# Kernel tuning notes

Hardware: AMD Instinct MI355X
Metric: run time of the kernel (lower is better)

The kernel has to match this reference:

```python
import jax, jax.numpy as jnp
import numpy as np

EMBED_DIM = 1024
NUM_HEADS = 16


def setup_inputs() -> dict:
    key = jax.random.key(0)
    kq, kk, kv = jax.random.split(key, 3)
    N, L, S, E = 4, 2048, 2048, EMBED_DIM
    return {
        "query": jax.random.normal(kq, (N, L, E), dtype=jnp.float32),
        "key": jax.random.normal(kk, (N, S, E), dtype=jnp.float32),
        "value": jax.random.normal(kv, (N, S, E), dtype=jnp.float32),
        "is_causal": 1,
    }


def reference(query, key, value, is_causal):
    N, L, E = query.shape
    _, S, E_v = value.shape
    H = NUM_HEADS
    dh = E // H
    dh_v = E_v // H
    # (N, H, L, dh) layout
    q = query.reshape(N, L, H, dh).transpose(0, 2, 1, 3)
    k = key.reshape(N, S, H, dh).transpose(0, 2, 1, 3)
    v = value.reshape(N, S, H, dh_v).transpose(0, 2, 1, 3)

    scale = 1.0 / np.sqrt(dh).astype(np.float32)
    # full LxS score matrix, as in the original (non-flash)
    scores = jnp.einsum('nhld,nhsd->nhls', q, k) * scale
    if is_causal:
        causal = jnp.tril(jnp.ones((L, S), dtype=bool))  # True = allowed
        scores = jnp.where(causal, scores, jnp.float32(-jnp.inf))
    attn_weight = jax.nn.softmax(scores, axis=-1)  # (N,H,L,S)
    y = jnp.einsum('nhls,nhsd->nhld', attn_weight, v)
    y = y.transpose(0, 2, 1, 3).reshape(N, L, E_v)
    return (y, attn_weight)
```

## Files before the change

### kernel.cpp

```cpp
#include <hip/hip_runtime.h>
#include <math.h>
#include <stdint.h>

#define N_B 4
#define N_H 16
#define L_Q 2048
#define L_K 2048
#define E_D 1024
#define DH  64
#define QB  128
#define KB  64
#define NT  512
#define NQT (L_Q / QB)
#define NKT (L_K / KB)
#define LDP  72
#define LDPV 68

typedef _Float16 f16x2 __attribute__((ext_vector_type(2)));
typedef _Float16 f16x4 __attribute__((ext_vector_type(4)));
typedef _Float16 f16x8 __attribute__((ext_vector_type(8)));
typedef float    f32x4 __attribute__((ext_vector_type(4)));

__device__ __forceinline__ f16x4 pk4(float a, float b, float c, float d) {
    f16x2 lo = __builtin_bit_cast(f16x2, __builtin_amdgcn_cvt_pkrtz(a, b));
    f16x2 hi = __builtin_bit_cast(f16x2, __builtin_amdgcn_cvt_pkrtz(c, d));
    f16x4 r; r[0] = lo[0]; r[1] = lo[1]; r[2] = hi[0]; r[3] = hi[1];
    return r;
}

__device__ __forceinline__ void gload16(const _Float16* g, _Float16* l) {
    __builtin_amdgcn_global_load_lds(
        (const __attribute__((address_space(1))) void*)g,
        (__attribute__((address_space(3))) void*)l, 16, 0, 0);
}

__global__ __launch_bounds__(256)
void cvt_qk(const float* __restrict__ Q, const float* __restrict__ K,
            _Float16* __restrict__ Qh, _Float16* __restrict__ Kh)
{
    size_t i = ((size_t)blockIdx.x * 256 + threadIdx.x) * 8;
    float4 a = *(const float4*)(Q + i);
    float4 b = *(const float4*)(Q + i + 4);
    *(f16x4*)(Qh + i)     = pk4(a.x, a.y, a.z, a.w);
    *(f16x4*)(Qh + i + 4) = pk4(b.x, b.y, b.z, b.w);
    float4 c = *(const float4*)(K + i);
    float4 d = *(const float4*)(K + i + 4);
    *(f16x4*)(Kh + i)     = pk4(c.x, c.y, c.z, c.w);
    *(f16x4*)(Kh + i + 4) = pk4(d.x, d.y, d.z, d.w);
}

__global__ __launch_bounds__(256)
void cvt_vt(const float* __restrict__ V, _Float16* __restrict__ Vt)
{
    __shared__ _Float16 T[64][72];
    const int bid = blockIdx.x;
    const int st  = bid & 31;
    const int nh  = bid >> 5;
    const int n   = nh >> 4;
    const int h   = nh & 15;
    const int t   = threadIdx.x;
    const float* Vb = V + ((size_t)(n * L_K + st * 64)) * E_D + h * DH;
    #pragma unroll
    for (int i = 0; i < 4; ++i) {
        int lin = t + i * 256;
        int s = lin >> 4, d = (lin & 15) * 4;
        float4 v = *(const float4*)(Vb + (size_t)s * E_D + d);
        T[d + 0][s] = (_Float16)v.x; T[d + 1][s] = (_Float16)v.y;
        T[d + 2][s] = (_Float16)v.z; T[d + 3][s] = (_Float16)v.w;
    }
    __syncthreads();
    _Float16* Ob = Vt + ((size_t)nh * DH) * L_K + st * 64;
    #pragma unroll
    for (int j = 0; j < 2; ++j) {
        int lin = t + j * 256;
        int d = lin >> 3, sc = (lin & 7) * 8;
        *(f16x8*)(Ob + (size_t)d * L_K + sc) = *(const f16x8*)&T[d][sc];
    }
}

__global__ __launch_bounds__(NT)
void mha_main(const _Float16* __restrict__ Qh, const _Float16* __restrict__ Kh,
              const _Float16* __restrict__ Vth, const int* __restrict__ causp,
              float* __restrict__ Yg, float* __restrict__ Wg)
{
    __shared__ __attribute__((aligned(16))) _Float16 KsL[2][KB * DH];
    __shared__ __attribute__((aligned(16))) _Float16 VsL[2][DH * KB];
    __shared__ __attribute__((aligned(16))) _Float16 Ps[QB][LDP];
    __shared__ float linv[QB];

    const int tid  = threadIdx.x;
    const int lane = tid & 63;
    const int wid  = tid >> 6;
    const int bid0 = blockIdx.x;
    const int bid  = ((bid0 & 7) << 7) + (bid0 >> 3);
    const int qt   = bid & (NQT - 1);
    const int nh   = bid >> 4;
    const int q0   = qt * QB;
    const int n    = nh >> 4;
    const int h    = nh & 15;
    const bool causal = (*causp) != 0;
    const float scale = 0.125f;

    const int lrow = lane & 15;
    const int g    = lane >> 4;
    const int rb   = wid * 16;
    const int rsub = g * 4;
    const int kt_end = causal ? (2 * qt + 2) : NKT;

    float*  Ybase = Yg + ((size_t)(n * L_Q + q0)) * E_D + h * DH;
    float*  Wbase = Wg + ((size_t)nh * L_Q + q0) * L_K;

    const int srow = wid * 8 + (lane >> 3);
    const int scol = (((lane & 7) ^ ((lane >> 3) & 7)) << 3);
    const _Float16* Ksrc0 = Kh  + ((size_t)(n * L_K) + srow) * E_D + h * DH + scol;
    const _Float16* Vsrc0 = Vth + ((size_t)nh * DH + srow) * L_K + scol;

    const int swz = (lrow & 7) << 4;
    const int cb0 = ((g * 16) ^ swz) >> 1;
    const int cb1 = ((64 + g * 16) ^ swz) >> 1;

    const _Float16* Qrow = Qh + ((size_t)(n * L_Q + q0 + rb + lrow)) * E_D + h * DH;
    const f16x8 qf0 = *(const f16x8*)(Qrow + g * 8);
    const f16x8 qf1 = *(const f16x8*)(Qrow + 32 + g * 8);

    #define STAGE_K(b, kt) gload16(Ksrc0 + (size_t)(kt) * KB * E_D, &KsL[b][wid * 512])
    #define STAGE_V(b, kt) gload16(Vsrc0 + (size_t)(kt) * KB,       &VsL[b][wid * 512])
    #define FRAG(buf, tc, half) (*(const f16x8*)&(buf)[(size_t)((tc) * 16 + lrow) * 64 + ((half) ? cb1 : cb0)])

    float l_part = 0.0f;
    STAGE_K(0, 0);
    __syncthreads();
    for (int kt = 0; kt < kt_end; ++kt) {
        const int cur = kt & 1;
        if (kt + 1 < kt_end) STAGE_K(cur ^ 1, kt + 1);

        f32x4 acc[4] = {};
        #pragma unroll
        for (int tc = 0; tc < 4; ++tc) {
            acc[tc] = __builtin_amdgcn_mfma_f32_16x16x32_f16(FRAG(KsL[cur], tc, 0), qf0, acc[tc], 0, 0, 0);
            acc[tc] = __builtin_amdgcn_mfma_f32_16x16x32_f16(FRAG(KsL[cur], tc, 1), qf1, acc[tc], 0, 0, 0);
        }
        const bool dm = causal && (kt >= 2 * qt);
        const int krel = (kt - 2 * qt) * 64;
        #pragma unroll
        for (int tc = 0; tc < 4; ++tc) {
            #pragma unroll
            for (int i = 0; i < 4; ++i) {
                float v = acc[tc][i] * scale;
                bool ok = !dm || (krel + tc * 16 + rsub + i <= rb + lrow);
                l_part += ok ? __expf(v) : 0.0f;
            }
        }
        __syncthreads();
    }
    l_part += __shfl_xor(l_part, 16);
    l_part += __shfl_xor(l_part, 32);
    const float inv_l = 1.0f / l_part;
    linv[rb + lrow] = inv_l;

    f32x4 o[4] = {};
    STAGE_K(0, 0);
    STAGE_V(0, 0);
    __syncthreads();

    float winv[4];
    #pragma unroll
    for (int j = 0; j < 4; ++j) winv[j] = linv[rb + (lane >> 4) + 4 * j];

    for (int kt = 0; kt < kt_end; ++kt) {
        const int cur = kt & 1;
        if (kt + 1 < kt_end) { STAGE_K(cur ^ 1, kt + 1); STAGE_V(cur ^ 1, kt + 1); }

        f32x4 acc[4] = {};
        #pragma unroll
        for (int tc = 0; tc < 4; ++tc) {
            acc[tc] = __builtin_amdgcn_mfma_f32_16x16x32_f16(FRAG(KsL[cur], tc, 0), qf0, acc[tc], 0, 0, 0);
            acc[tc] = __builtin_amdgcn_mfma_f32_16x16x32_f16(FRAG(KsL[cur], tc, 1), qf1, acc[tc], 0, 0, 0);
        }

        const bool dm = causal && (kt >= 2 * qt);
        const int krel = (kt - 2 * qt) * 64;
        #pragma unroll
        for (int tc = 0; tc < 4; ++tc) {
            float v, p0, p1, p2, p3;
            v = acc[tc][0] * scale;
            p0 = (!dm || (krel + tc * 16 + rsub + 0 <= rb + lrow)) ? __expf(v) : 0.0f;
            v = acc[tc][1] * scale;
            p1 = (!dm || (krel + tc * 16 + rsub + 1 <= rb + lrow)) ? __expf(v) : 0.0f;
            v = acc[tc][2] * scale;
            p2 = (!dm || (krel + tc * 16 + rsub + 2 <= rb + lrow)) ? __expf(v) : 0.0f;
            v = acc[tc][3] * scale;
            p3 = (!dm || (krel + tc * 16 + rsub + 3 <= rb + lrow)) ? __expf(v) : 0.0f;
            *(f16x4*)&Ps[rb + lrow][tc * 16 + rsub] = pk4(p0, p1, p2, p3);
        }

        f16x8 pf0 = *(const f16x8*)&Ps[rb + lrow][0 + g * 8];
        f16x8 pf1 = *(const f16x8*)&Ps[rb + lrow][32 + g * 8];
        #pragma unroll
        for (int tc = 0; tc < 4; ++tc) {
            o[tc] = __builtin_amdgcn_mfma_f32_16x16x32_f16(FRAG(VsL[cur], tc, 0), pf0, o[tc], 0, 0, 0);
            o[tc] = __builtin_amdgcn_mfma_f32_16x16x32_f16(FRAG(VsL[cur], tc, 1), pf1, o[tc], 0, 0, 0);
        }

        {
            float* Wt = Wbase + (size_t)kt * KB;
            const int c0 = (lane & 15) * 4;
            #pragma unroll
            for (int j = 0; j < 4; ++j) {
                const int rl = rb + (lane >> 4) + 4 * j;
                f16x4 pv = *(const f16x4*)&Ps[rl][c0];
                const float s = winv[j];
                float4 wv = make_float4((float)pv[0] * s, (float)pv[1] * s,
                                        (float)pv[2] * s, (float)pv[3] * s);
                *(float4*)(Wt + (size_t)rl * L_K + c0) = wv;
            }
        }

        __builtin_amdgcn_sched_barrier(0);
        asm volatile("s_waitcnt vmcnt(4) lgkmcnt(0)" ::: "memory");
        __builtin_amdgcn_s_barrier();
        __builtin_amdgcn_sched_barrier(0);
    }

    #pragma unroll
    for (int tc = 0; tc < 4; ++tc) {
        float4 yv = make_float4(o[tc][0] * inv_l, o[tc][1] * inv_l,
                                o[tc][2] * inv_l, o[tc][3] * inv_l);
        *(float4*)(Ybase + (size_t)(rb + lrow) * E_D + tc * 16 + rsub) = yv;
    }

    if (causal && kt_end < NKT) {
        const int c0 = kt_end * KB;
        const int rem4 = (L_K - c0) >> 2;
        const float4 z = make_float4(0.f, 0.f, 0.f, 0.f);
        for (int r = 0; r < QB; ++r) {
            float* row = Wbase + (size_t)r * L_K + c0;
            for (int c4 = tid; c4 < rem4; c4 += NT) {
                *(float4*)(row + c4 * 4) = z;
            }
        }
    }
    #undef STAGE_K
    #undef STAGE_V
    #undef FRAG
}

__global__ __launch_bounds__(256)
void mha_fwd_fallback(const float* __restrict__ Qg, const float* __restrict__ Kg,
                      const float* __restrict__ Vg, const int* __restrict__ causp,
                      float* __restrict__ Yg, float* __restrict__ Wg)
{
    __shared__ __attribute__((aligned(16))) _Float16 Qs[64][LDP];
    __shared__ __attribute__((aligned(16))) _Float16 Ks[64][LDP];
    __shared__ __attribute__((aligned(16))) _Float16 Psf[64][LDP];
    __shared__ __attribute__((aligned(16))) _Float16 Vt[DH][LDPV];

    const int tid  = threadIdx.x;
    const int lane = tid & 63;
    const int wid  = tid >> 6;
    const int bid  = blockIdx.x;
    const int qt   = bid & 31;
    const int nh   = bid >> 5;
    const int q0   = qt * 64;
    const int n    = nh >> 4;
    const int h    = nh & 15;
    const bool causal = (*causp) != 0;
    const float scale = 0.125f;

    const float* Qbase = Qg + ((size_t)(n * L_Q + q0)) * E_D + h * DH;
    const float* Kbase = Kg + ((size_t)n * L_K) * E_D + h * DH;
    const float* Vbase = Vg + ((size_t)n * L_K) * E_D + h * DH;
    float*       Ybase = Yg + ((size_t)(n * L_Q + q0)) * E_D + h * DH;
    float*       Wbase = Wg + ((size_t)nh * L_Q + q0) * L_K;

    const int lrow = lane & 15;
    const int lk   = (lane >> 4) * 8;
    const int rb   = wid * 16;
    const int rsub = (lane >> 4) * 4;
    const int kt_end = causal ? (qt + 1) : NKT;

    #pragma unroll
    for (int i = 0; i < 4; ++i) {
        int lin = tid + i * 256;
        int r = lin >> 4;
        int c = (lin & 15) * 4;
        float4 qv = *(const float4*)(Qbase + (size_t)r * E_D + c);
        *(f16x4*)&Qs[r][c] = pk4(qv.x, qv.y, qv.z, qv.w);
    }
    __syncthreads();
    const f16x8 qf0 = *(const f16x8*)&Qs[rb + lrow][lk];
    const f16x8 qf1 = *(const f16x8*)&Qs[rb + lrow][32 + lk];

    float l_part = 0.0f;
    for (int kt = 0; kt < kt_end; ++kt) {
        const float* Kt = Kbase + (size_t)kt * KB * E_D;
        __syncthreads();
        #pragma unroll
        for (int i = 0; i < 4; ++i) {
            int lin = tid + i * 256;
            int r = lin >> 4;
            int c = (lin & 15) * 4;
            float4 kv = *(const float4*)(Kt + (size_t)r * E_D + c);
            *(f16x4*)&Ks[r][c] = pk4(kv.x, kv.y, kv.z, kv.w);
        }
        __syncthreads();
        f32x4 acc[4] = {};
        #pragma unroll
        for (int tc = 0; tc < 4; ++tc) {
            f16x8 a0 = *(const f16x8*)&Ks[tc * 16 + lrow][lk];
            f16x8 a1 = *(const f16x8*)&Ks[tc * 16 + lrow][32 + lk];
            acc[tc] = __builtin_amdgcn_mfma_f32_16x16x32_f16(a0, qf0, acc[tc], 0, 0, 0);
            acc[tc] = __builtin_amdgcn_mfma_f32_16x16x32_f16(a1, qf1, acc[tc], 0, 0, 0);
        }
        const bool dm = causal && (kt == qt);
        #pragma unroll
        for (int tc = 0; tc < 4; ++tc) {
            #pragma unroll
            for (int i = 0; i < 4; ++i) {
                float v = acc[tc][i] * scale;
                bool ok = !dm || (tc * 16 + rsub + i <= rb + lrow);
                l_part += ok ? __expf(v) : 0.0f;
            }
        }
    }
    l_part += __shfl_xor(l_part, 16);
    l_part += __shfl_xor(l_part, 32);
    const float inv_l = 1.0f / l_part;

    f32x4 o[4] = {};
    for (int kt = 0; kt < kt_end; ++kt) {
        const float* Kt  = Kbase + (size_t)kt * KB * E_D;
        const float* Vtg = Vbase + (size_t)kt * KB * E_D;
        __syncthreads();
        #pragma unroll
        for (int i = 0; i < 4; ++i) {
            int lin = tid + i * 256;
            int r = lin >> 4;
            int c = (lin & 15) * 4;
            float4 kv = *(const float4*)(Kt + (size_t)r * E_D + c);
            *(f16x4*)&Ks[r][c] = pk4(kv.x, kv.y, kv.z, kv.w);
            int d   = lin & 63;
            int kk0 = (lin >> 6) * 4;
            float v0 = Vtg[(size_t)(kk0 + 0) * E_D + d];
            float v1 = Vtg[(size_t)(kk0 + 1) * E_D + d];
            float v2 = Vtg[(size_t)(kk0 + 2) * E_D + d];
            float v3 = Vtg[(size_t)(kk0 + 3) * E_D + d];
            *(f16x4*)&Vt[d][kk0] = pk4(v0, v1, v2, v3);
        }
        __syncthreads();
        f32x4 acc[4] = {};
        #pragma unroll
        for (int tc = 0; tc < 4; ++tc) {
            f16x8 a0 = *(const f16x8*)&Ks[tc * 16 + lrow][lk];
            f16x8 a1 = *(const f16x8*)&Ks[tc * 16 + lrow][32 + lk];
            acc[tc] = __builtin_amdgcn_mfma_f32_16x16x32_f16(a0, qf0, acc[tc], 0, 0, 0);
            acc[tc] = __builtin_amdgcn_mfma_f32_16x16x32_f16(a1, qf1, acc[tc], 0, 0, 0);
        }
        const bool dm = causal && (kt == qt);
        float* Wrow = Wbase + (size_t)(rb + lrow) * L_K + kt * KB;
        #pragma unroll
        for (int tc = 0; tc < 4; ++tc) {
            float v, p0, p1, p2, p3;
            v = acc[tc][0] * scale;
            p0 = (!dm || (tc * 16 + rsub + 0 <= rb + lrow)) ? __expf(v) : 0.0f;
            v = acc[tc][1] * scale;
            p1 = (!dm || (tc * 16 + rsub + 1 <= rb + lrow)) ? __expf(v) : 0.0f;
            v = acc[tc][2] * scale;
            p2 = (!dm || (tc * 16 + rsub + 2 <= rb + lrow)) ? __expf(v) : 0.0f;
            v = acc[tc][3] * scale;
            p3 = (!dm || (tc * 16 + rsub + 3 <= rb + lrow)) ? __expf(v) : 0.0f;
            float4 wv = make_float4(p0 * inv_l, p1 * inv_l, p2 * inv_l, p3 * inv_l);
            *(float4*)(Wrow + tc * 16 + rsub) = wv;
            *(f16x4*)&Psf[rb + lrow][tc * 16 + rsub] = pk4(p0, p1, p2, p3);
        }
        f16x8 pf0 = *(const f16x8*)&Psf[rb + lrow][lk];
        f16x8 pf1 = *(const f16x8*)&Psf[rb + lrow][32 + lk];
        #pragma unroll
        for (int tc = 0; tc < 4; ++tc) {
            f16x4 t0 = *(const f16x4*)&Vt[tc * 16 + lrow][lk];
            f16x4 t1 = *(const f16x4*)&Vt[tc * 16 + lrow][lk + 4];
            f16x8 a0 = __builtin_shufflevector(t0, t1, 0, 1, 2, 3, 4, 5, 6, 7);
            f16x4 t2 = *(const f16x4*)&Vt[tc * 16 + lrow][32 + lk];
            f16x4 t3 = *(const f16x4*)&Vt[tc * 16 + lrow][32 + lk + 4];
            f16x8 a1 = __builtin_shufflevector(t2, t3, 0, 1, 2, 3, 4, 5, 6, 7);
            o[tc] = __builtin_amdgcn_mfma_f32_16x16x32_f16(a0, pf0, o[tc], 0, 0, 0);
            o[tc] = __builtin_amdgcn_mfma_f32_16x16x32_f16(a1, pf1, o[tc], 0, 0, 0);
        }
    }
    #pragma unroll
    for (int tc = 0; tc < 4; ++tc) {
        float4 yv = make_float4(o[tc][0] * inv_l, o[tc][1] * inv_l,
                                o[tc][2] * inv_l, o[tc][3] * inv_l);
        *(float4*)(Ybase + (size_t)(rb + lrow) * E_D + tc * 16 + rsub) = yv;
    }
    if (causal && kt_end < NKT) {
        const int c0 = kt_end * KB;
        const int rem4 = (L_K - c0) >> 2;
        const float4 z = make_float4(0.f, 0.f, 0.f, 0.f);
        for (int r = 0; r < 64; ++r) {
            float* row = Wbase + (size_t)r * L_K + c0;
            for (int c4 = tid; c4 < rem4; c4 += 256) {
                *(float4*)(row + c4 * 4) = z;
            }
        }
    }
}

extern "C" void kernel_launch(void* const* d_in, const int* in_sizes, int n_in,
                              void* d_out, int out_size, void* d_ws, size_t ws_size,
                              hipStream_t stream) {
    const float* Q  = (const float*)d_in[0];
    const float* K  = (const float*)d_in[1];
    const float* V  = (const float*)d_in[2];
    const int* caus = (const int*)d_in[3];
    float* Y = (float*)d_out;
    float* W = (float*)d_out + (size_t)N_B * L_Q * E_D;

    const size_t elems = (size_t)N_B * L_Q * E_D;
    const size_t need  = 3 * elems * sizeof(_Float16);

    if (ws_size >= need) {
        _Float16* Qh = (_Float16*)d_ws;
        _Float16* Kh = Qh + elems;
        _Float16* Vt = Kh + elems;
        hipLaunchKernelGGL(cvt_qk, dim3(elems / (256 * 8)), dim3(256), 0, stream, Q, K, Qh, Kh);
        hipLaunchKernelGGL(cvt_vt, dim3(N_B * N_H * (L_K / 64)), dim3(256), 0, stream, V, Vt);
        hipLaunchKernelGGL(mha_main, dim3(N_B * N_H * NQT), dim3(NT), 0, stream,
                           Qh, Kh, Vt, caus, Y, W);
    } else {
        hipLaunchKernelGGL(mha_fwd_fallback, dim3(N_B * N_H * 32), dim3(256), 0, stream,
                           Q, K, V, caus, Y, W);
    }
}
```

Measured before the change: 328.3 us.

## Reverse q-tile order, pair K tiles in row-sum pass, use nontemporal stores

Three changes. Query tiles are now assigned in reverse, so the causal blocks with the most K tiles get scheduled first, which helps load balance. The first (row-sum) pass stages two K tiles per barrier, borrowing the V buffer as a second slot, which halves the number of barriers. The output and attention-weight stores, including the zero fill, become nontemporal to cut cache pollution on the large write stream. The pairing assumes kt_end is even; under the causal setting it is 2*qt+2, and in the non-causal case it is 32.

```diff
diff --git a/kernel.cpp b/kernel.cpp
--- a/kernel.cpp
+++ b/kernel.cpp
@@ -93,7 +93,7 @@
     const int wid  = tid >> 6;
     const int bid0 = blockIdx.x;
     const int bid  = ((bid0 & 7) << 7) + (bid0 >> 3);
-    const int qt   = bid & (NQT - 1);
+    const int qt   = (NQT - 1) - (bid & (NQT - 1));
     const int nh   = bid >> 4;
     const int q0   = qt * QB;
     const int n    = nh >> 4;
@@ -124,31 +124,45 @@
     const f16x8 qf1 = *(const f16x8*)(Qrow + 32 + g * 8);
 
     #define STAGE_K(b, kt) gload16(Ksrc0 + (size_t)(kt) * KB * E_D, &KsL[b][wid * 512])
+    #define STAGE_KV(b, kt) gload16(Ksrc0 + (size_t)(kt) * KB * E_D, &VsL[b][wid * 512])
     #define STAGE_V(b, kt) gload16(Vsrc0 + (size_t)(kt) * KB,       &VsL[b][wid * 512])
     #define FRAG(buf, tc, half) (*(const f16x8*)&(buf)[(size_t)((tc) * 16 + lrow) * 64 + ((half) ? cb1 : cb0)])
 
     float l_part = 0.0f;
-    STAGE_K(0, 0);
-    __syncthreads();
-    for (int kt = 0; kt < kt_end; ++kt) {
-        const int cur = kt & 1;
-        if (kt + 1 < kt_end) STAGE_K(cur ^ 1, kt + 1);
-
-        f32x4 acc[4] = {};
-        #pragma unroll
-        for (int tc = 0; tc < 4; ++tc) {
-            acc[tc] = __builtin_amdgcn_mfma_f32_16x16x32_f16(FRAG(KsL[cur], tc, 0), qf0, acc[tc], 0, 0, 0);
-            acc[tc] = __builtin_amdgcn_mfma_f32_16x16x32_f16(FRAG(KsL[cur], tc, 1), qf1, acc[tc], 0, 0, 0);
-        }
-        const bool dm = causal && (kt >= 2 * qt);
-        const int krel = (kt - 2 * qt) * 64;
-        #pragma unroll
-        for (int tc = 0; tc < 4; ++tc) {
+    {
+        const int np = kt_end >> 1;
+        STAGE_K(0, 0);
+        STAGE_KV(0, 1);
+        for (int p = 0; p < np; ++p) {
+            __builtin_amdgcn_sched_barrier(0);
+            asm volatile("s_waitcnt vmcnt(0) lgkmcnt(0)" ::: "memory");
+            __builtin_amdgcn_s_barrier();
+            __builtin_amdgcn_sched_barrier(0);
+            if (p + 1 < np) {
+                STAGE_K((p + 1) & 1, 2 * p + 2);
+                STAGE_KV((p + 1) & 1, 2 * p + 3);
+            }
             #pragma unroll
-            for (int i = 0; i < 4; ++i) {
-                float v = acc[tc][i] * scale;
-                bool ok = !dm || (krel + tc * 16 + rsub + i <= rb + lrow);
-                l_part += ok ? __expf(v) : 0.0f;
+            for (int half = 0; half < 2; ++half) {
+                const int kt = 2 * p + half;
+                const _Float16* Kc = half ? &VsL[p & 1][0] : &KsL[p & 1][0];
+                f32x4 acc[4] = {};
+                #pragma unroll
+                for (int tc = 0; tc < 4; ++tc) {
+                    acc[tc] = __builtin_amdgcn_mfma_f32_16x16x32_f16(FRAG(Kc, tc, 0), qf0, acc[tc], 0, 0, 0);
+                    acc[tc] = __builtin_amdgcn_mfma_f32_16x16x32_f16(FRAG(Kc, tc, 1), qf1, acc[tc], 0, 0, 0);
+                }
+                const bool dm = causal && (kt >= 2 * qt);
+                const int krel = (kt - 2 * qt) * 64;
+                #pragma unroll
+                for (int tc = 0; tc < 4; ++tc) {
+                    #pragma unroll
+                    for (int i = 0; i < 4; ++i) {
+                        float v = acc[tc][i] * scale;
+                        bool ok = !dm || (krel + tc * 16 + rsub + i <= rb + lrow);
+                        l_part += ok ? __expf(v) : 0.0f;
+                    }
+                }
             }
         }
         __syncthreads();
@@ -210,9 +224,9 @@
                 const int rl = rb + (lane >> 4) + 4 * j;
                 f16x4 pv = *(const f16x4*)&Ps[rl][c0];
                 const float s = winv[j];
-                float4 wv = make_float4((float)pv[0] * s, (float)pv[1] * s,
-                                        (float)pv[2] * s, (float)pv[3] * s);
-                *(float4*)(Wt + (size_t)rl * L_K + c0) = wv;
+                f32x4 wv = { (float)pv[0] * s, (float)pv[1] * s,
+                             (float)pv[2] * s, (float)pv[3] * s };
+                __builtin_nontemporal_store(wv, (f32x4*)(Wt + (size_t)rl * L_K + c0));
             }
         }
 
@@ -224,23 +238,24 @@
 
     #pragma unroll
     for (int tc = 0; tc < 4; ++tc) {
-        float4 yv = make_float4(o[tc][0] * inv_l, o[tc][1] * inv_l,
-                                o[tc][2] * inv_l, o[tc][3] * inv_l);
-        *(float4*)(Ybase + (size_t)(rb + lrow) * E_D + tc * 16 + rsub) = yv;
+        f32x4 yv = { o[tc][0] * inv_l, o[tc][1] * inv_l,
+                     o[tc][2] * inv_l, o[tc][3] * inv_l };
+        __builtin_nontemporal_store(yv, (f32x4*)(Ybase + (size_t)(rb + lrow) * E_D + tc * 16 + rsub));
     }
 
     if (causal && kt_end < NKT) {
         const int c0 = kt_end * KB;
         const int rem4 = (L_K - c0) >> 2;
-        const float4 z = make_float4(0.f, 0.f, 0.f, 0.f);
+        const f32x4 z = { 0.f, 0.f, 0.f, 0.f };
         for (int r = 0; r < QB; ++r) {
             float* row = Wbase + (size_t)r * L_K + c0;
             for (int c4 = tid; c4 < rem4; c4 += NT) {
-                *(float4*)(row + c4 * 4) = z;
+                __builtin_nontemporal_store(z, (f32x4*)(row + c4 * 4));
             }
         }
     }
     #undef STAGE_K
+    #undef STAGE_KV
     #undef STAGE_V
     #undef FRAG
 }
```

Result: faster. 276.1 us (-15.9%).
